# Optimization experiments

Measured on AMD Instinct MI355X. Metric: run time of the kernel, lower is better.

The kernel has to match this reference:

```python
import jax, jax.numpy as jnp
import numpy as np
from jax import lax

B, T = 256, 64
X_DIMS, CCG_DIMS, H, N_TAG = 512, 256, 1024, 512
DIN = X_DIMS + CCG_DIMS
PAD = 0


def setup_inputs() -> dict:
    key = jax.random.key(0)
    ks = jax.random.split(key, 12)
    emb = jax.random.normal(ks[0], (N_TAG, CCG_DIMS), jnp.float32)
    emb = emb.at[PAD].set(0.0)  # padding_idx row is zero
    s_ih = 1.0 / np.sqrt(H)
    return {
        "x": jax.random.normal(ks[1], (B, X_DIMS), jnp.float32),
        "atom_truth": jax.random.randint(ks[2], (B, T), 0, N_TAG),
        "atom_mask": jax.random.randint(ks[3], (B, T), 0, 2).astype(bool),
        "emb": emb,
        "W_ih": jax.random.normal(ks[4], (4 * H, DIN), jnp.float32) * s_ih,
        "W_hh": jax.random.normal(ks[5], (4 * H, H), jnp.float32) * s_ih,
        "b_ih": jax.random.normal(ks[6], (4 * H,), jnp.float32) * s_ih,
        "b_hh": jax.random.normal(ks[7], (4 * H,), jnp.float32) * s_ih,
        "W_out": jax.random.normal(ks[8], (N_TAG, H), jnp.float32) * s_ih,
        "b_out": jax.random.normal(ks[9], (N_TAG,), jnp.float32) * s_ih,
        "h0": jax.random.normal(ks[10], (B, H), jnp.float32),
        "c0": jax.random.normal(ks[11], (B, H), jnp.float32),
    }


def reference(x, atom_truth, atom_mask, emb, W_ih, W_hh, b_ih, b_hh, W_out, b_out, h0, c0):
    b, t = atom_truth.shape
    # teacher forcing: step 0 uses token 0, step k uses atom_truth[:, k-1]
    prev_tok = jnp.concatenate([jnp.zeros((b, 1), atom_truth.dtype), atom_truth[:, :-1]], axis=1)
    ccg = emb[prev_tok]                                      # [B,T,E]
    inp = jnp.concatenate([jnp.broadcast_to(x[:, None, :], (b, t, x.shape[1])), ccg], axis=-1)
    # precompute input projection for all steps: [B,T,4H]
    xproj = jnp.einsum('btd,gd->btg', inp, W_ih) + b_ih + b_hh

    def cell(carry, xt):                                     # xt: [B,4H]
        h, c = carry
        gates = xt + h @ W_hh.T
        i, f, g, o = jnp.split(gates, 4, axis=-1)            # torch gate order i,f,g,o
        i, f, o = jax.nn.sigmoid(i), jax.nn.sigmoid(f), jax.nn.sigmoid(o)
        g = jnp.tanh(g)
        c = f * c + i * g
        h = o * jnp.tanh(c)
        return (h, c), h

    _, hs = lax.scan(cell, (h0, c0), jnp.swapaxes(xproj, 0, 1))  # hs: [T,B,H]
    logits = hs @ W_out.T + b_out                            # [T,B,N_TAG]
    logp = jax.nn.log_softmax(logits, axis=-1)
    tgt = atom_truth.T                                       # [T,B]
    nll = -jnp.take_along_axis(logp, tgt[..., None], axis=-1)[..., 0]  # [T,B]
    mask = atom_mask.T.astype(nll.dtype)
    return jnp.sum(nll * mask) / jnp.sum(mask)


if __name__ == "__main__":
    print(reference(**setup_inputs()))
```

## Files before the change

kernel.cpp:

```cpp
#include <hip/hip_runtime.h>
#include <hip/hip_bf16.h>

#define BB 256
#define TT 64
#define XD 512
#define CCG 256
#define DINk 768
#define HH 1024
#define G4 4096
#define NTAG 512

typedef float f32x4 __attribute__((ext_vector_type(4)));
typedef short s16x8 __attribute__((ext_vector_type(8)));
typedef short s16x4 __attribute__((ext_vector_type(4)));

#define WS_HS    0ull
#define WS_XBASE (WS_HS + (size_t)(TT+1)*BB*HH*2)
#define WS_EPROJ (WS_XBASE + (size_t)BB*G4*4)
#define WS_WIH   (WS_EPROJ + (size_t)NTAG*G4*4)
#define WS_WOUT  (WS_WIH + (size_t)G4*DINk*2)
#define WS_XBF   (WS_WOUT + (size_t)NTAG*HH*2)
#define WS_EMBBF (WS_XBF + (size_t)BB*XD*2)
#define WS_CNT   (WS_EMBBF + (size_t)NTAG*CCG*2)
#define WS_ACC   (WS_CNT + 4096)
#define WS_FLAG  (WS_ACC + 64)
#define WS_XPROJ (WS_FLAG + 64)

static __device__ __forceinline__ short f2bf(float f) {
  __hip_bfloat16 h = __float2bfloat16(f);
  return __builtin_bit_cast(short, h);
}
static __device__ __forceinline__ float bf2f(unsigned short u) {
  unsigned x = ((unsigned)u) << 16;
  return __builtin_bit_cast(float, x);
}
static __device__ __forceinline__ void store_dword_cc(void* p, unsigned v) {
  asm volatile("global_store_dword %0, %1, off sc0 sc1" :: "v"(p), "v"(v) : "memory");
}
static __device__ __forceinline__ void store_short_cc(void* p, unsigned v) {
  asm volatile("global_store_short %0, %1, off sc0 sc1" :: "v"(p), "v"(v) : "memory");
}
static __device__ __forceinline__ int4 load_int4_cc(const void* p) {
  int4 r;
  asm volatile("global_load_dwordx4 %0, %1, off sc0 sc1\n\ts_waitcnt vmcnt(0)"
               : "=v"(r) : "v"(p) : "memory");
  return r;
}
static __device__ __forceinline__ float fsig(float x) {
  return __builtin_amdgcn_rcpf(1.f + __expf(-x));
}
static __device__ __forceinline__ float ftanh(float x) {
  return 1.f - 2.f * __builtin_amdgcn_rcpf(1.f + __expf(2.f * x));
}

__global__ void k_f2bf8(const float* __restrict__ in, short* __restrict__ out, int n8) {
  int i = blockIdx.x * blockDim.x + threadIdx.x;
  if (i >= n8) return;
  size_t idx = (size_t)i * 8;
  float4 a = *(const float4*)(in + idx);
  float4 b = *(const float4*)(in + idx + 4);
  s16x8 o;
  o[0]=f2bf(a.x); o[1]=f2bf(a.y); o[2]=f2bf(a.z); o[3]=f2bf(a.w);
  o[4]=f2bf(b.x); o[5]=f2bf(b.y); o[6]=f2bf(b.z); o[7]=f2bf(b.w);
  *(s16x8*)(out + idx) = o;
}

__global__ void k_init(const float* __restrict__ h0, const int* __restrict__ mask_as_int,
                       char* __restrict__ ws) {
  int tid = blockIdx.x * blockDim.x + threadIdx.x;
  short* hb0 = (short*)(ws + WS_HS);
  for (int i = tid; i < BB * HH; i += gridDim.x * blockDim.x) hb0[i] = f2bf(h0[i]);
  if (blockIdx.x == 0) {
    int* cnt = (int*)(ws + WS_CNT);
    for (int i = threadIdx.x; i < 1024; i += blockDim.x) cnt[i] = 0;
    int v = 0;
    for (int i = threadIdx.x; i < 4096; i += blockDim.x) v |= (mask_as_int[i] & ~1);
    __shared__ int red[256];
    red[threadIdx.x] = v;
    __syncthreads();
    if (threadIdx.x == 0) {
      int a = 0;
      for (int j = 0; j < 256; j++) a |= red[j];
      ((int*)(ws + WS_FLAG))[0] = (a != 0) ? 1 : 0;
      float* acc = (float*)(ws + WS_ACC);
      acc[0] = 0.f; acc[1] = 0.f;
    }
  }
}

__global__ __launch_bounds__(256) void k_gemm(const short* __restrict__ A, int lda,
    const short* __restrict__ Bm, int ldb, int bcol0,
    short* __restrict__ C, int ldc, int ksteps,
    const float* __restrict__ bias1, const float* __restrict__ bias2) {
  int w = threadIdx.x >> 6, l = threadIdx.x & 63;
  int lc = l & 15, lq = l >> 4;
  int arow = blockIdx.x * 64 + w * 16 + lc;
  f32x4 acc[4];
  const f32x4 z = {0.f, 0.f, 0.f, 0.f};
#pragma unroll
  for (int i = 0; i < 4; i++) acc[i] = z;
  const short* ap = A + (size_t)arow * lda + lq * 8;
  for (int kk = 0; kk < ksteps; ++kk) {
    s16x8 a = *(const s16x8*)(ap + kk * 32);
#pragma unroll
    for (int nt = 0; nt < 4; ++nt) {
      int brow = blockIdx.y * 64 + nt * 16 + lc;
      s16x8 b = *(const s16x8*)(Bm + (size_t)brow * ldb + bcol0 + kk * 32 + lq * 8);
      acc[nt] = __builtin_amdgcn_mfma_f32_16x16x32_bf16(a, b, acc[nt], 0, 0, 0);
    }
  }
#pragma unroll
  for (int nt = 0; nt < 4; ++nt) {
    int col = blockIdx.y * 64 + nt * 16 + lc;
    float badd = (bias1 ? bias1[col] : 0.f) + (bias2 ? bias2[col] : 0.f);
#pragma unroll
    for (int j = 0; j < 4; j++) {
      int r = blockIdx.x * 64 + w * 16 + lq * 4 + j;
      C[(size_t)r * ldc + col] = f2bf(acc[nt][j] + badd);
    }
  }
}

__global__ __launch_bounds__(256) void k_xproj_t(const short* __restrict__ xb,
    const short* __restrict__ ep, const int* __restrict__ atruth,
    short* __restrict__ out) {
  __shared__ short tile[64 * 264];
  const int cc = blockIdx.x, g = blockIdx.y, t = blockIdx.z;
  const int b = threadIdx.x;
  const int tok = (t == 0) ? 0 : atruth[b * TT + t - 1];
  const int gc0 = g * 1024 + cc * 64;
  const short* xs = xb + (size_t)b * G4 + gc0;
  const short* es = ep + (size_t)tok * G4 + gc0;
#pragma unroll
  for (int i = 0; i < 64; i += 8) {
    s16x8 xv = *(const s16x8*)(xs + i);
    s16x8 ev = *(const s16x8*)(es + i);
#pragma unroll
    for (int j = 0; j < 8; ++j)
      tile[(i + j) * 264 + b] = f2bf(bf2f((unsigned short)xv[j]) + bf2f((unsigned short)ev[j]));
  }
  __syncthreads();
  const int c = threadIdx.x >> 2, b0 = (threadIdx.x & 3) * 64;
  short* dst = out + ((size_t)t * G4 + gc0 + c) * BB + b0;
  const short* src = tile + c * 264 + b0;
#pragma unroll
  for (int i = 0; i < 64; i += 8) *(s16x8*)(dst + i) = *(const s16x8*)(src + i);
}

__global__ __launch_bounds__(512, 2) void k_lstm(const float* __restrict__ Whh,
    const short* __restrict__ xproj, const float* __restrict__ c0,
    char* __restrict__ ws) {
  extern __shared__ char sm[];
  float* part = (float*)(sm + 131072);
  const int bid = blockIdx.x;
  const int xcd = bid & 7, slot = bid >> 3;
  const int mg = xcd >> 1;
  const int hb = slot * 2 + (xcd & 1);
  const int wgid = (xcd & 1) * 32 + slot;
  const int tid = threadIdx.x;
  const int w = tid >> 6, l = tid & 63;
  const int lc = l & 15, lq = l >> 4;
  const int wy = w & 3, kh = w >> 2;

  {
    const int r = tid >> 3, q = tid & 7;
    const int g = r >> 4, rl = r & 15;
    const float* src = Whh + (size_t)(g * HH + hb * 16 + rl) * HH + q * 128;
    const int swz = (rl & 7) << 4;
    char* dst = sm + r * 2048;
#pragma unroll
    for (int i = 0; i < 128; i += 8) {
      float4 f0 = *(const float4*)(src + i);
      float4 f1 = *(const float4*)(src + i + 4);
      s16x8 o;
      o[0]=f2bf(f0.x); o[1]=f2bf(f0.y); o[2]=f2bf(f0.z); o[3]=f2bf(f0.w);
      o[4]=f2bf(f1.x); o[5]=f2bf(f1.y); o[6]=f2bf(f1.z); o[7]=f2bf(f1.w);
      int koff = (q * 128 + i) * 2;
      *(s16x8*)(dst + (koff ^ swz)) = o;
    }
  }

  const int colbase = hb * 16;
  short* hs = (short*)(ws + WS_HS);
  int* flags4 = (int*)(ws + WS_CNT);
  const int swzl = (lc & 7) << 4;
  const int row0 = mg * 64 + wy * 16;

  float cst[4];
  if (kh == 0) {
#pragma unroll
    for (int j = 0; j < 4; ++j)
      cst[j] = c0[(size_t)(row0 + lq * 4 + j) * HH + colbase + lc];
  }
  float* pslot = part + ((size_t)wy * 64 + l) * 20;
  __syncthreads();

  for (int t = 0; t < TT; ++t) {
    s16x4 xg[4];
    if (kh == 0) {
#pragma unroll
      for (int g = 0; g < 4; ++g)
        xg[g] = *(const s16x4*)(xproj +
            ((size_t)t * G4 + g * HH + colbase + lc) * BB + row0 + lq * 4);
    }

    if (t && w == 0) {
      const int4* f = (const int4*)flags4 + (mg * 64 + l);
      for (;;) {
        int4 v = load_int4_cc(f);
        if (__all((v.x >= t) && (v.y >= t) && (v.z >= t) && (v.w >= t))) break;
        __builtin_amdgcn_s_sleep(1);
      }
    }
    __syncthreads();

    const f32x4 z = {0.f, 0.f, 0.f, 0.f};
    f32x4 acc0 = z, acc1 = z, acc2 = z, acc3 = z;
    const short* arowp = hs + (size_t)t * (BB * HH) + (size_t)(row0 + lc) * HH + kh * 512 + lq * 8;
#pragma unroll
    for (int kk = 0; kk < 16; ++kk) {
      s16x8 a = *(const s16x8*)(arowp + kk * 32);
      const int kx = (((kh * 16 + kk) * 64) + lq * 16) ^ swzl;
      const char* bp = sm + lc * 2048 + kx;
      acc0 = __builtin_amdgcn_mfma_f32_16x16x32_bf16(a, *(const s16x8*)(bp), acc0, 0, 0, 0);
      acc1 = __builtin_amdgcn_mfma_f32_16x16x32_bf16(a, *(const s16x8*)(bp + 16 * 2048), acc1, 0, 0, 0);
      acc2 = __builtin_amdgcn_mfma_f32_16x16x32_bf16(a, *(const s16x8*)(bp + 32 * 2048), acc2, 0, 0, 0);
      acc3 = __builtin_amdgcn_mfma_f32_16x16x32_bf16(a, *(const s16x8*)(bp + 48 * 2048), acc3, 0, 0, 0);
    }

    if (kh == 1) {
      *(f32x4*)(pslot) = acc0;
      *(f32x4*)(pslot + 4) = acc1;
      *(f32x4*)(pslot + 8) = acc2;
      *(f32x4*)(pslot + 12) = acc3;
    }
    __syncthreads();

    if (kh == 0) {
      acc0 += *(const f32x4*)(pslot);
      acc1 += *(const f32x4*)(pslot + 4);
      acc2 += *(const f32x4*)(pslot + 8);
      acc3 += *(const f32x4*)(pslot + 12);
      short* hrow = hs + (size_t)(t + 1) * (BB * HH) +
                    (size_t)(row0 + lq * 4) * HH + colbase + lc;
#pragma unroll
      for (int j = 0; j < 4; ++j) {
        float pi = acc0[j] + bf2f((unsigned short)xg[0][j]);
        float pf = acc1[j] + bf2f((unsigned short)xg[1][j]);
        float pg = acc2[j] + bf2f((unsigned short)xg[2][j]);
        float po = acc3[j] + bf2f((unsigned short)xg[3][j]);
        float cv = fsig(pf) * cst[j] + fsig(pi) * ftanh(pg);
        cst[j] = cv;
        store_short_cc(hrow + (size_t)j * HH, (unsigned)(unsigned short)f2bf(fsig(po) * ftanh(cv)));
      }
      asm volatile("s_waitcnt vmcnt(0)" ::: "memory");
      if (l == 0 && t < TT - 1)
        store_dword_cc(flags4 + (mg * 64 + wgid) * 4 + wy, t + 1);
    }
  }
}

__global__ __launch_bounds__(256, 1) void k_logits(const short* __restrict__ hsb,
    const short* __restrict__ Wo, const float* __restrict__ bout,
    const int* __restrict__ atruth, const void* __restrict__ maskp,
    char* __restrict__ ws) {
  extern __shared__ char sm[];
  const int tid = threadIdx.x;
  const int w = tid >> 6, l = tid & 63;
  const int lc = l & 15, lq = l >> 4;
  const int rowbase = blockIdx.x * 64 + w * 16;
  f32x4 acc[32];
#pragma unroll
  for (int nt = 0; nt < 32; ++nt) {
    float bv = bout[nt * 16 + lc];
    f32x4 tmp = {bv, bv, bv, bv};
    acc[nt] = tmp;
  }
  const int swzl = (lc & 7) << 4;
  for (int kb = 0; kb < 16; ++kb) {
    __syncthreads();
    {
      const int r0 = tid >> 3, q = tid & 7;
#pragma unroll
      for (int i = 0; i < 16; i++) {
        int r = r0 + 32 * i;
        s16x8 v = *(const s16x8*)(Wo + (size_t)r * HH + kb * 64 + q * 8);
        *(s16x8*)(sm + r * 128 + ((q * 16) ^ ((r & 7) << 4))) = v;
      }
    }
    __syncthreads();
#pragma unroll
    for (int ks = 0; ks < 2; ++ks) {
      s16x8 a = *(const s16x8*)(hsb + (size_t)(rowbase + lc) * HH + kb * 64 + ks * 32 + lq * 8);
      const int kx = (ks * 64 + lq * 16) ^ swzl;
#pragma unroll
      for (int nt = 0; nt < 32; ++nt) {
        s16x8 b = *(const s16x8*)(sm + (nt * 16 + lc) * 128 + kx);
        acc[nt] = __builtin_amdgcn_mfma_f32_16x16x32_bf16(a, b, acc[nt], 0, 0, 0);
      }
    }
  }
  const int bytemode = ((const int*)(ws + WS_FLAG))[0];
  const unsigned char* mb = (const unsigned char*)maskp;
  const int* mi = (const int*)maskp;
  float nlls = 0.f, cnts = 0.f;
#pragma unroll
  for (int j = 0; j < 4; j++) {
    int gr = rowbase + lq * 4 + j;
    int tt = gr >> 8, b = gr & 255;
    float m = -1e30f;
#pragma unroll
    for (int nt = 0; nt < 32; ++nt) m = fmaxf(m, acc[nt][j]);
    m = fmaxf(m, __shfl_xor(m, 1)); m = fmaxf(m, __shfl_xor(m, 2));
    m = fmaxf(m, __shfl_xor(m, 4)); m = fmaxf(m, __shfl_xor(m, 8));
    float s = 0.f;
#pragma unroll
    for (int nt = 0; nt < 32; ++nt) s += __expf(acc[nt][j] - m);
    s += __shfl_xor(s, 1); s += __shfl_xor(s, 2);
    s += __shfl_xor(s, 4); s += __shfl_xor(s, 8);
    float lse = m + __logf(s);
    int tg = atruth[b * TT + tt];
    int mk = bytemode ? (int)mb[b * TT + tt] : mi[b * TT + tt];
    if (((tg & 15) == lc) && mk) {
      float tl = 0.f;
#pragma unroll
      for (int nt = 0; nt < 32; ++nt) if (nt == (tg >> 4)) tl = acc[nt][j];
      nlls += (lse - tl);
    }
    if (lc == 0 && mk) cnts += 1.f;
  }
#pragma unroll
  for (int off = 1; off < 64; off <<= 1) {
    nlls += __shfl_xor(nlls, off);
    cnts += __shfl_xor(cnts, off);
  }
  if (l == 0) {
    float* accf = (float*)(ws + WS_ACC);
    atomicAdd(&accf[0], nlls);
    atomicAdd(&accf[1], cnts);
  }
}

__global__ void k_final(const char* __restrict__ ws, float* __restrict__ out) {
  const float* accf = (const float*)(ws + WS_ACC);
  out[0] = accf[0] / accf[1];
}

extern "C" void kernel_launch(void* const* d_in, const int* in_sizes, int n_in,
                              void* d_out, int out_size, void* d_ws, size_t ws_size,
                              hipStream_t stream) {
  const float* x      = (const float*)d_in[0];
  const int*   atruth = (const int*)d_in[1];
  const void*  amask  = d_in[2];
  const float* emb    = (const float*)d_in[3];
  const float* W_ih   = (const float*)d_in[4];
  const float* W_hh   = (const float*)d_in[5];
  const float* b_ih   = (const float*)d_in[6];
  const float* b_hh   = (const float*)d_in[7];
  const float* W_out  = (const float*)d_in[8];
  const float* b_out  = (const float*)d_in[9];
  const float* h0     = (const float*)d_in[10];
  const float* c0     = (const float*)d_in[11];
  char* ws = (char*)d_ws;
  float* out = (float*)d_out;

  hipFuncSetAttribute((const void*)k_lstm, hipFuncAttributeMaxDynamicSharedMemorySize, 151552);
  hipFuncSetAttribute((const void*)k_logits, hipFuncAttributeMaxDynamicSharedMemorySize, 65536);

  k_f2bf8<<<dim3((G4 * DINk / 8 + 255) / 256), 256, 0, stream>>>(W_ih, (short*)(ws + WS_WIH), G4 * DINk / 8);
  k_f2bf8<<<dim3((NTAG * HH / 8 + 255) / 256), 256, 0, stream>>>(W_out, (short*)(ws + WS_WOUT), NTAG * HH / 8);
  k_f2bf8<<<dim3((BB * XD / 8 + 255) / 256), 256, 0, stream>>>(x, (short*)(ws + WS_XBF), BB * XD / 8);
  k_f2bf8<<<dim3((NTAG * CCG / 8 + 255) / 256), 256, 0, stream>>>(emb, (short*)(ws + WS_EMBBF), NTAG * CCG / 8);

  k_init<<<64, 256, 0, stream>>>(h0, (const int*)amask, ws);

  k_gemm<<<dim3(4, 64), 256, 0, stream>>>((short*)(ws + WS_XBF), XD, (short*)(ws + WS_WIH), DINk, 0,
                                          (short*)(ws + WS_XBASE), G4, XD / 32, b_ih, b_hh);
  k_gemm<<<dim3(8, 64), 256, 0, stream>>>((short*)(ws + WS_EMBBF), CCG, (short*)(ws + WS_WIH), DINk, XD,
                                          (short*)(ws + WS_EPROJ), G4, CCG / 32, nullptr, nullptr);

  k_xproj_t<<<dim3(16, 4, 64), 256, 0, stream>>>((const short*)(ws + WS_XBASE),
                                                 (const short*)(ws + WS_EPROJ), atruth,
                                                 (short*)(ws + WS_XPROJ));

  k_lstm<<<256, 512, 151552, stream>>>(W_hh, (const short*)(ws + WS_XPROJ), c0, ws);

  k_logits<<<256, 256, 65536, stream>>>((short*)(ws + WS_HS) + BB * HH, (short*)(ws + WS_WOUT), b_out,
                                        atruth, amask, ws);
  k_final<<<1, 1, 0, stream>>>(ws, out);
}
```

Measured before the change: 625.4 us.

## Split LSTM batch into two interleaved groups to overlap sync with compute

```diff
diff --git a/kernel.cpp b/kernel.cpp
--- a/kernel.cpp
+++ b/kernel.cpp
@@ -40,9 +40,9 @@
 static __device__ __forceinline__ void store_short_cc(void* p, unsigned v) {
   asm volatile("global_store_short %0, %1, off sc0 sc1" :: "v"(p), "v"(v) : "memory");
 }
-static __device__ __forceinline__ int4 load_int4_cc(const void* p) {
-  int4 r;
-  asm volatile("global_load_dwordx4 %0, %1, off sc0 sc1\n\ts_waitcnt vmcnt(0)"
+static __device__ __forceinline__ int2 load_int2_cc(const void* p) {
+  int2 r;
+  asm volatile("global_load_dwordx2 %0, %1, off sc0 sc1\n\ts_waitcnt vmcnt(0)"
                : "=v"(r) : "v"(p) : "memory");
   return r;
 }
@@ -147,20 +147,21 @@
   for (int i = 0; i < 64; i += 8) *(s16x8*)(dst + i) = *(const s16x8*)(src + i);
 }
 
-__global__ __launch_bounds__(512, 2) void k_lstm(const float* __restrict__ Whh,
+__global__ __launch_bounds__(512) void k_lstm(const float* __restrict__ Whh,
     const short* __restrict__ xproj, const float* __restrict__ c0,
     char* __restrict__ ws) {
   extern __shared__ char sm[];
   float* part = (float*)(sm + 131072);
   const int bid = blockIdx.x;
   const int xcd = bid & 7, slot = bid >> 3;
-  const int mg = xcd >> 1;
+  const int p = xcd >> 1;
   const int hb = slot * 2 + (xcd & 1);
-  const int wgid = (xcd & 1) * 32 + slot;
+  const int colbase = hb * 16;
+  const int gA = p, gB = p + 4;
   const int tid = threadIdx.x;
   const int w = tid >> 6, l = tid & 63;
   const int lc = l & 15, lq = l >> 4;
-  const int wy = w & 3, kh = w >> 2;
+  const int wy = w & 1, kq = w >> 1;
 
   {
     const int r = tid >> 3, q = tid & 7;
@@ -180,82 +181,191 @@
     }
   }
 
-  const int colbase = hb * 16;
   short* hs = (short*)(ws + WS_HS);
-  int* flags4 = (int*)(ws + WS_CNT);
+  int* flags = (int*)(ws + WS_CNT);
   const int swzl = (lc & 7) << 4;
-  const int row0 = mg * 64 + wy * 16;
-
-  float cst[4];
-  if (kh == 0) {
+  const int rA0 = gA * 32 + wy * 16;
+  const int rB0 = gB * 32 + wy * 16;
+
+  float cstA[4], cstB[4];
+  s16x4 xgA[4], xnA[4], xgB[4], xnB[4];
+  if (kq == 0) {
 #pragma unroll
     for (int j = 0; j < 4; ++j)
-      cst[j] = c0[(size_t)(row0 + lq * 4 + j) * HH + colbase + lc];
-  }
-  float* pslot = part + ((size_t)wy * 64 + l) * 20;
+      cstA[j] = c0[(size_t)(rA0 + lq * 4 + j) * HH + colbase + lc];
+#pragma unroll
+    for (int g = 0; g < 4; ++g)
+      asm volatile("global_load_dwordx2 %0, %1, off" : "=v"(xgA[g])
+        : "v"(xproj + ((size_t)g * HH + colbase + lc) * BB + rA0 + lq * 4));
+  }
+  if (kq == 1) {
+#pragma unroll
+    for (int j = 0; j < 4; ++j)
+      cstB[j] = c0[(size_t)(rB0 + lq * 4 + j) * HH + colbase + lc];
+#pragma unroll
+    for (int g = 0; g < 4; ++g)
+      asm volatile("global_load_dwordx2 %0, %1, off" : "=v"(xgB[g])
+        : "v"(xproj + ((size_t)g * HH + colbase + lc) * BB + rB0 + lq * 4));
+  }
   __syncthreads();
 
   for (int t = 0; t < TT; ++t) {
-    s16x4 xg[4];
-    if (kh == 0) {
+    if (t && w == 0) {
+      const int2* f = (const int2*)flags + gA * 64 + l;
+      for (;;) {
+        int2 v = load_int2_cc(f);
+        if (__all((v.x >= t) && (v.y >= t))) break;
+        __builtin_amdgcn_s_sleep(1);
+      }
+    }
+    __syncthreads();
+
+    if (kq == 0 && t + 1 < TT) {
+      const short* xp = xproj + ((size_t)(t + 1) * G4 + colbase + lc) * BB + rA0 + lq * 4;
 #pragma unroll
       for (int g = 0; g < 4; ++g)
-        xg[g] = *(const s16x4*)(xproj +
-            ((size_t)t * G4 + g * HH + colbase + lc) * BB + row0 + lq * 4);
-    }
-
-    if (t && w == 0) {
-      const int4* f = (const int4*)flags4 + (mg * 64 + l);
-      for (;;) {
-        int4 v = load_int4_cc(f);
-        if (__all((v.x >= t) && (v.y >= t) && (v.z >= t) && (v.w >= t))) break;
-        __builtin_amdgcn_s_sleep(1);
-      }
-    }
-    __syncthreads();
-
+        asm volatile("global_load_dwordx2 %0, %1, off" : "=v"(xnA[g]) : "v"(xp + (size_t)g * HH * BB));
+    }
+    s16x8 af[8];
+    {
+      const short* ap = hs + (size_t)t * (BB * HH) + (size_t)(rA0 + lc) * HH + kq * 256 + lq * 8;
+#pragma unroll
+      for (int kk = 0; kk < 8; ++kk)
+        asm volatile("global_load_dwordx4 %0, %1, off" : "=v"(af[kk]) : "v"(ap + kk * 32));
+      asm volatile("s_waitcnt vmcnt(0)" ::: "memory");
+    }
     const f32x4 z = {0.f, 0.f, 0.f, 0.f};
     f32x4 acc0 = z, acc1 = z, acc2 = z, acc3 = z;
-    const short* arowp = hs + (size_t)t * (BB * HH) + (size_t)(row0 + lc) * HH + kh * 512 + lq * 8;
-#pragma unroll
-    for (int kk = 0; kk < 16; ++kk) {
-      s16x8 a = *(const s16x8*)(arowp + kk * 32);
-      const int kx = (((kh * 16 + kk) * 64) + lq * 16) ^ swzl;
+#pragma unroll
+    for (int kk = 0; kk < 8; ++kk) {
+      const int kx = (kq * 512 + kk * 64 + lq * 16) ^ swzl;
       const char* bp = sm + lc * 2048 + kx;
-      acc0 = __builtin_amdgcn_mfma_f32_16x16x32_bf16(a, *(const s16x8*)(bp), acc0, 0, 0, 0);
-      acc1 = __builtin_amdgcn_mfma_f32_16x16x32_bf16(a, *(const s16x8*)(bp + 16 * 2048), acc1, 0, 0, 0);
-      acc2 = __builtin_amdgcn_mfma_f32_16x16x32_bf16(a, *(const s16x8*)(bp + 32 * 2048), acc2, 0, 0, 0);
-      acc3 = __builtin_amdgcn_mfma_f32_16x16x32_bf16(a, *(const s16x8*)(bp + 48 * 2048), acc3, 0, 0, 0);
-    }
-
-    if (kh == 1) {
-      *(f32x4*)(pslot) = acc0;
-      *(f32x4*)(pslot + 4) = acc1;
-      *(f32x4*)(pslot + 8) = acc2;
-      *(f32x4*)(pslot + 12) = acc3;
-    }
-    __syncthreads();
-
-    if (kh == 0) {
-      acc0 += *(const f32x4*)(pslot);
-      acc1 += *(const f32x4*)(pslot + 4);
-      acc2 += *(const f32x4*)(pslot + 8);
-      acc3 += *(const f32x4*)(pslot + 12);
-      short* hrow = hs + (size_t)(t + 1) * (BB * HH) +
-                    (size_t)(row0 + lq * 4) * HH + colbase + lc;
+      acc0 = __builtin_amdgcn_mfma_f32_16x16x32_bf16(af[kk], *(const s16x8*)(bp), acc0, 0, 0, 0);
+      acc1 = __builtin_amdgcn_mfma_f32_16x16x32_bf16(af[kk], *(const s16x8*)(bp + 16 * 2048), acc1, 0, 0, 0);
+      acc2 = __builtin_amdgcn_mfma_f32_16x16x32_bf16(af[kk], *(const s16x8*)(bp + 32 * 2048), acc2, 0, 0, 0);
+      acc3 = __builtin_amdgcn_mfma_f32_16x16x32_bf16(af[kk], *(const s16x8*)(bp + 48 * 2048), acc3, 0, 0, 0);
+    }
+    if (kq != 0) {
+      float* ps = part + (((size_t)wy * 3 + (kq - 1)) * 16) * 64 + l;
 #pragma unroll
       for (int j = 0; j < 4; ++j) {
-        float pi = acc0[j] + bf2f((unsigned short)xg[0][j]);
-        float pf = acc1[j] + bf2f((unsigned short)xg[1][j]);
-        float pg = acc2[j] + bf2f((unsigned short)xg[2][j]);
-        float po = acc3[j] + bf2f((unsigned short)xg[3][j]);
-        float cv = fsig(pf) * cst[j] + fsig(pi) * ftanh(pg);
-        cst[j] = cv;
+        ps[(0 * 4 + j) * 64] = acc0[j];
+        ps[(1 * 4 + j) * 64] = acc1[j];
+        ps[(2 * 4 + j) * 64] = acc2[j];
+        ps[(3 * 4 + j) * 64] = acc3[j];
+      }
+    }
+    if (t && w == 2) {
+      const int2* f = (const int2*)flags + gB * 64 + l;
+      for (;;) {
+        int2 v = load_int2_cc(f);
+        if (__all((v.x >= t) && (v.y >= t))) break;
+        __builtin_amdgcn_s_sleep(1);
+      }
+    }
+    __syncthreads();
+
+    s16x8 bf[8];
+    {
+      const short* bp2 = hs + (size_t)t * (BB * HH) + (size_t)(rB0 + lc) * HH + kq * 256 + lq * 8;
+#pragma unroll
+      for (int kk = 0; kk < 8; ++kk)
+        asm volatile("global_load_dwordx4 %0, %1, off" : "=v"(bf[kk]) : "v"(bp2 + kk * 32));
+    }
+    if (kq == 1 && t + 1 < TT) {
+      const short* xp = xproj + ((size_t)(t + 1) * G4 + colbase + lc) * BB + rB0 + lq * 4;
+#pragma unroll
+      for (int g = 0; g < 4; ++g)
+        asm volatile("global_load_dwordx2 %0, %1, off" : "=v"(xnB[g]) : "v"(xp + (size_t)g * HH * BB));
+    }
+    if (kq == 0) {
+#pragma unroll
+      for (int q = 0; q < 3; ++q) {
+        const float* ps = part + (((size_t)wy * 3 + q) * 16) * 64 + l;
+#pragma unroll
+        for (int j = 0; j < 4; ++j) {
+          acc0[j] += ps[(0 * 4 + j) * 64];
+          acc1[j] += ps[(1 * 4 + j) * 64];
+          acc2[j] += ps[(2 * 4 + j) * 64];
+          acc3[j] += ps[(3 * 4 + j) * 64];
+        }
+      }
+    }
+    __syncthreads();
+
+    if (kq == 0) {
+      short* hrow = hs + (size_t)(t + 1) * (BB * HH) + (size_t)(rA0 + lq * 4) * HH + colbase + lc;
+#pragma unroll
+      for (int j = 0; j < 4; ++j) {
+        float pi = acc0[j] + bf2f((unsigned short)xgA[0][j]);
+        float pf = acc1[j] + bf2f((unsigned short)xgA[1][j]);
+        float pg = acc2[j] + bf2f((unsigned short)xgA[2][j]);
+        float po = acc3[j] + bf2f((unsigned short)xgA[3][j]);
+        float cv = fsig(pf) * cstA[j] + fsig(pi) * ftanh(pg);
+        cstA[j] = cv;
         store_short_cc(hrow + (size_t)j * HH, (unsigned)(unsigned short)f2bf(fsig(po) * ftanh(cv)));
       }
       asm volatile("s_waitcnt vmcnt(0)" ::: "memory");
       if (l == 0 && t < TT - 1)
-        store_dword_cc(flags4 + (mg * 64 + wgid) * 4 + wy, t + 1);
+        store_dword_cc(flags + (gA * 64 + hb) * 2 + wy, t + 1);
+      xgA[0] = xnA[0]; xgA[1] = xnA[1]; xgA[2] = xnA[2]; xgA[3] = xnA[3];
+    }
+
+    asm volatile("s_waitcnt vmcnt(0)" ::: "memory");
+    f32x4 bcc0 = z, bcc1 = z, bcc2 = z, bcc3 = z;
+#pragma unroll
+    for (int kk = 0; kk < 8; ++kk) {
+      const int kx = (kq * 512 + kk * 64 + lq * 16) ^ swzl;
+      const char* bp = sm + lc * 2048 + kx;
+      bcc0 = __builtin_amdgcn_mfma_f32_16x16x32_bf16(bf[kk], *(const s16x8*)(bp), bcc0, 0, 0, 0);
+      bcc1 = __builtin_amdgcn_mfma_f32_16x16x32_bf16(bf[kk], *(const s16x8*)(bp + 16 * 2048), bcc1, 0, 0, 0);
+      bcc2 = __builtin_amdgcn_mfma_f32_16x16x32_bf16(bf[kk], *(const s16x8*)(bp + 32 * 2048), bcc2, 0, 0, 0);
+      bcc3 = __builtin_amdgcn_mfma_f32_16x16x32_bf16(bf[kk], *(const s16x8*)(bp + 48 * 2048), bcc3, 0, 0, 0);
+    }
+    if (kq != 1) {
+      const int q = (kq == 0) ? 0 : kq - 1;
+      float* ps = part + (((size_t)wy * 3 + q) * 16) * 64 + l;
+#pragma unroll
+      for (int j = 0; j < 4; ++j) {
+        ps[(0 * 4 + j) * 64] = bcc0[j];
+        ps[(1 * 4 + j) * 64] = bcc1[j];
+        ps[(2 * 4 + j) * 64] = bcc2[j];
+        ps[(3 * 4 + j) * 64] = bcc3[j];
+      }
+    }
+    __syncthreads();
+
+    if (kq == 1) {
+#pragma unroll
+      for (int q = 0; q < 3; ++q) {
+        const float* ps = part + (((size_t)wy * 3 + q) * 16) * 64 + l;
+#pragma unroll
+        for (int j = 0; j < 4; ++j) {
+          bcc0[j] += ps[(0 * 4 + j) * 64];
+          bcc1[j] += ps[(1 * 4 + j) * 64];
+          bcc2[j] += ps[(2 * 4 + j) * 64];
+          bcc3[j] += ps[(3 * 4 + j) * 64];
+        }
+      }
+    }
+    __syncthreads();
+
+    if (kq == 1) {
+      short* hrow = hs + (size_t)(t + 1) * (BB * HH) + (size_t)(rB0 + lq * 4) * HH + colbase + lc;
+#pragma unroll
+      for (int j = 0; j < 4; ++j) {
+        float pi = bcc0[j] + bf2f((unsigned short)xgB[0][j]);
+        float pf = bcc1[j] + bf2f((unsigned short)xgB[1][j]);
+        float pg = bcc2[j] + bf2f((unsigned short)xgB[2][j]);
+        float po = bcc3[j] + bf2f((unsigned short)xgB[3][j]);
+        float cv = fsig(pf) * cstB[j] + fsig(pi) * ftanh(pg);
+        cstB[j] = cv;
+        store_short_cc(hrow + (size_t)j * HH, (unsigned)(unsigned short)f2bf(fsig(po) * ftanh(cv)));
+      }
+      asm volatile("s_waitcnt vmcnt(0)" ::: "memory");
+      if (l == 0 && t < TT - 1)
+        store_dword_cc(flags + (gB * 64 + hb) * 2 + wy, t + 1);
+      xgB[0] = xnB[0]; xgB[1] = xnB[1]; xgB[2] = xnB[2]; xgB[3] = xnB[3];
     }
   }
 }
@@ -364,7 +474,7 @@
   char* ws = (char*)d_ws;
   float* out = (float*)d_out;
 
-  hipFuncSetAttribute((const void*)k_lstm, hipFuncAttributeMaxDynamicSharedMemorySize, 151552);
+  hipFuncSetAttribute((const void*)k_lstm, hipFuncAttributeMaxDynamicSharedMemorySize, 155648);
   hipFuncSetAttribute((const void*)k_logits, hipFuncAttributeMaxDynamicSharedMemorySize, 65536);
 
   k_f2bf8<<<dim3((G4 * DINk / 8 + 255) / 256), 256, 0, stream>>>(W_ih, (short*)(ws + WS_WIH), G4 * DINk / 8);
@@ -383,7 +493,7 @@
                                                  (const short*)(ws + WS_EPROJ), atruth,
                                                  (short*)(ws + WS_XPROJ));
 
-  k_lstm<<<256, 512, 151552, stream>>>(W_hh, (const short*)(ws + WS_XPROJ), c0, ws);
+  k_lstm<<<256, 512, 155648, stream>>>(W_hh, (const short*)(ws + WS_XPROJ), c0, ws);
 
   k_logits<<<256, 256, 65536, stream>>>((short*)(ws + WS_HS) + BB * HH, (short*)(ws + WS_WOUT), b_out,
                                         atruth, amask, ws);
```

Result: slower. 706.5 us (+13.0%).
